# Optimization experiments

Measured on AMD Instinct MI355X. Metric: run time of the kernel, lower is better.

Reference implementation:

```python
import jax, jax.numpy as jnp
import numpy as np

B, T, D = 32, 256, 256  # batch, input_length, output_dim (input_dim == output_dim)
SCALE = 0.06  # ~ 1/sqrt(D) glorot-ish init so LSTM gates don't saturate


def hard_sigmoid(x):
    # Keras-1 default inner_activation for LSTM
    return jnp.clip(0.2 * x + 0.5, 0.0, 1.0)


def lstm_cell(x_t, h, c, W, U, b, d):
    # Keras gate order: i, f, c(g), o
    z = x_t @ W + h @ U + b
    i = hard_sigmoid(z[:, :d])
    f = hard_sigmoid(z[:, d:2 * d])
    g = jnp.tanh(z[:, 2 * d:3 * d])
    o = hard_sigmoid(z[:, 3 * d:])
    c_new = f * c + i * g
    h_new = o * jnp.tanh(c_new)
    return h_new, c_new


def setup_inputs() -> dict:
    key = jax.random.key(0)
    ks = jax.random.split(key, 7)
    x = jax.random.normal(ks[0], (B, T, D), dtype=jnp.float32)
    reader_W = jax.random.normal(ks[1], (D, 4 * D), dtype=jnp.float32) * SCALE
    reader_U = jax.random.normal(ks[2], (D, 4 * D), dtype=jnp.float32) * SCALE
    reader_b = jnp.zeros((4 * D,), jnp.float32)
    writer_W = jax.random.normal(ks[3], (2 * D, 4 * D), dtype=jnp.float32) * SCALE
    writer_U = jax.random.normal(ks[4], (D, 4 * D), dtype=jnp.float32) * SCALE
    writer_b = jnp.zeros((4 * D,), jnp.float32)
    composer_W = jax.random.normal(ks[5], (2 * D, 2 * D), dtype=jnp.float32) * SCALE
    composer_b = jnp.zeros((2 * D,), jnp.float32)
    return {"x": x, "reader_W": reader_W, "reader_U": reader_U, "reader_b": reader_b,
            "writer_W": writer_W, "writer_U": writer_U, "writer_b": writer_b,
            "composer_W": composer_W, "composer_b": composer_b}


def reference(x, reader_W, reader_U, reader_b, writer_W, writer_U, writer_b,
              composer_W, composer_b):
    b, t, d = x.shape
    h0 = jnp.zeros((b, d), x.dtype)
    c0 = jnp.zeros((b, d), x.dtype)

    # ---- read: reader LSTM over the sequence (return_sequences) ----
    def rstep(carry, x_t):
        h, c = carry
        h, c = lstm_cell(x_t, h, c, reader_W, reader_U, reader_b, d)
        return (h, c), h

    _, o_seq = jax.lax.scan(rstep, (h0, c0), jnp.swapaxes(x, 0, 1))  # [T,B,D]

    mem0 = x  # mem_0 = input (B, T, D)

    # ---- compose_and_write_step per timestep ----
    def step(carry, o_t):
        mem, wh, wc = carry
        # summarize_memory: eqs 2-3
        scores = jnp.einsum('bd,btd->bt', o_t, mem)
        z_t = jax.nn.softmax(scores, axis=-1)                 # (B, T)
        m_rt = jnp.einsum('bt,btd->bd', z_t, mem)             # (B, D)
        # compose (eq 4), linear activation
        c_t = jnp.concatenate([o_t, m_rt], axis=-1) @ composer_W + composer_b  # (B, 2D)
        # writer LSTM step (eq 5)
        wh, wc = lstm_cell(c_t, wh, wc, writer_W, writer_U, writer_b, d)
        # update_memory (eq 6): blend via tiled z_t / h_t
        zt = z_t[:, :, None]
        mem = mem * (1.0 - zt) + wh[:, None, :] * zt
        return (mem, wh, wc), wh

    (_, _, _), hs = jax.lax.scan(step, (mem0, h0, c0), o_seq)  # hs: [T,B,D]
    return hs[-1]  # return_mode == 'last_output'
```

## Files before the change

kernel.cpp:

```cpp
#include <hip/hip_runtime.h>
#include <math.h>

#define TB 512
#define NBATCH 32
#define TT 256
#define DD 256

typedef float f32x4 __attribute__((ext_vector_type(4)));

#define WS_WF   0u
#define WS_BF   524288u
#define WS_HP   525312u
#define WS_PAR  541696u
#define PS      260
#define WS_WHP  608256u
#define WS_BAR  616448u
#define WS_FLOATS 624704u

#define O_WW    0
#define S_WW    792
#define O_RW    12672
#define S_RW    524
#define O_MEM   21056
#define S_MEM   260
#define O_WACT  29376
#define S_WACT  792
#define O_RACT  35712
#define S_RACT  524
#define O_WZ    39904
#define O_RZ    40064
#define O_SS    40224
#define O_SE    40256
#define O_WC    40288
#define O_RC    40320
#define O_WB    40352
#define O_RB    40368
#define O_RJ    40384
#define O_MS    40448
#define LDS_FLOATS 40576
#define DYN_LDS_BYTES (LDS_FLOATS*4)

__device__ __forceinline__ float hsig(float x) { return fminf(fmaxf(0.2f*x + 0.5f, 0.f), 1.f); }
__device__ __forceinline__ int ak(int k) { return k + 4*(k/128); }

__device__ __forceinline__ void gst(float* p, float v) {
  __hip_atomic_store(p, v, __ATOMIC_RELAXED, __HIP_MEMORY_SCOPE_AGENT);
}
__device__ __forceinline__ float gld(const float* p) {
  return __hip_atomic_load(p, __ATOMIC_RELAXED, __HIP_MEMORY_SCOPE_AGENT);
}
__device__ __forceinline__ void gst4(float* p, f32x4 v) {
  asm volatile("global_store_dwordx4 %0, %1, off sc0 sc1" :: "v"(p), "v"(v) : "memory");
}

__device__ __forceinline__ void bar_arrive(int* myflag, int phase) {
  asm volatile("s_waitcnt vmcnt(0) lgkmcnt(0)" ::: "memory");
  __syncthreads();
  if (threadIdx.x == 0)
    __hip_atomic_store(myflag, phase, __ATOMIC_RELAXED, __HIP_MEMORY_SCOPE_AGENT);
}
__device__ __forceinline__ void bar_wait(int* flags, int phase) {
  if (threadIdx.x < 64) {
    int sp = 0;
    for (;;) {
      const int v = __hip_atomic_load(&flags[threadIdx.x*32], __ATOMIC_RELAXED,
                                      __HIP_MEMORY_SCOPE_AGENT);
      if (__all(v >= phase)) break;
      if (++sp > (1 << 16)) break;
    }
  }
  __syncthreads();
}
__device__ __forceinline__ void barrier_fenced(int* cnt, int target) {
  __syncthreads();
  if (threadIdx.x == 0) {
    __threadfence();
    __hip_atomic_fetch_add(cnt, 1, __ATOMIC_RELAXED, __HIP_MEMORY_SCOPE_AGENT);
    int sp = 0;
    while (__hip_atomic_load(cnt, __ATOMIC_RELAXED, __HIP_MEMORY_SCOPE_AGENT) < target) {
      if (++sp > (1 << 20)) break;
    }
    __threadfence();
  }
  __syncthreads();
}

__global__ void __launch_bounds__(TB) nse_kernel(
    const float* __restrict__ x,
    const float* __restrict__ rW, const float* __restrict__ rU, const float* __restrict__ rb,
    const float* __restrict__ wW, const float* __restrict__ wU, const float* __restrict__ wb,
    const float* __restrict__ cW, const float* __restrict__ cb,
    float* __restrict__ out, float* __restrict__ ws)
{
  extern __shared__ float sm[];
  const int tid = threadIdx.x;
  const int w = blockIdx.x;
  const int g = w >> 6;
  const int m = w & 63;
  const int b0 = g * 8;
  const int blm = m >> 3;
  const int isl = m & 7;
  const int bmy = b0 + blm;

  float* Wf   = ws + WS_WF;
  float* bfv  = ws + WS_BF;
  float* hpub = ws + WS_HP;
  float* par  = ws + WS_PAR;
  float* whp  = ws + WS_WHP;
  int*   bars = (int*)(ws + WS_BAR);
  int* flg    = &bars[g*2048];
  int* myflag = &bars[g*2048 + m*32];
  int* lcnt   = &bars[8192];
  int* magic  = &bars[8192 + 32];

  if (w == 0 && tid == 0) {
    __hip_atomic_store(lcnt, 0, __ATOMIC_RELAXED, __HIP_MEMORY_SCOPE_AGENT);
    __hip_atomic_store(magic, 1357911, __ATOMIC_RELEASE, __HIP_MEMORY_SCOPE_AGENT);
  }
  if (tid == 0) {
    int sp = 0;
    while (__hip_atomic_load(magic, __ATOMIC_ACQUIRE, __HIP_MEMORY_SCOPE_AGENT) != 1357911) {
      if (++sp > (1 << 20)) break;
    }
  }
  __syncthreads();

  {
    const int kt = w >> 4, nt = w & 15;
    const int r = tid >> 4, c4 = (tid & 15) * 4;
    float a0 = 0.f, a1 = 0.f, a2 = 0.f, a3 = 0.f;
    for (int jc = 0; jc < 512; jc += 32) {
      for (int u = tid; u < 1024; u += TB) {
        int rr = u >> 5, jj = u & 31;
        sm[rr*33 + jj] = cW[(32*kt + rr)*512 + jc + jj];
      }
      {
        int jj = tid >> 4, cc = (tid & 15) * 4;
        const f32x4 v = *(const f32x4*)&wW[(jc + jj)*1024 + 64*nt + cc];
        float* d = &sm[1056 + jj*68 + cc];
        d[0] = v.x; d[1] = v.y; d[2] = v.z; d[3] = v.w;
      }
      __syncthreads();
      #pragma unroll 8
      for (int j = 0; j < 32; j++) {
        const float a = sm[r*33 + j];
        const float* wv = &sm[1056 + j*68 + c4];
        a0 += a*wv[0]; a1 += a*wv[1]; a2 += a*wv[2]; a3 += a*wv[3];
      }
      __syncthreads();
    }
    float* d = &Wf[(32*kt + r)*1024 + 64*nt + c4];
    d[0] = a0; d[1] = a1; d[2] = a2; d[3] = a3;
  }
  if (w >= 16 && w < 32) {
    __syncthreads();
    const int base = (w - 16) * 64;
    const int c = tid & 63, jq = tid >> 6;
    float p = 0.f;
    for (int j = 64*jq; j < 64*jq + 64; j++) p += cb[j] * wW[j*1024 + base + c];
    sm[jq*68 + c] = p;
    __syncthreads();
    if (tid < 64) {
      float s = wb[base + tid];
      for (int j = 0; j < 8; j++) s += sm[j*68 + tid];
      bfv[base + tid] = s;
    }
  }
  barrier_fenced(lcnt, 256);

  for (int u = tid; u < 3072; u += TB) {
    const int k = u >> 2, gate = u & 3;
    const float* sp = (k < 512) ? &Wf[(size_t)k*1024 + gate*256 + 4*m]
                                : &wU[(size_t)(k-512)*1024 + gate*256 + 4*m];
    const f32x4 v = *(const f32x4*)sp;
    const int ik = ak(k);
    sm[O_WW + (gate*4+0)*S_WW + ik] = v.x;
    sm[O_WW + (gate*4+1)*S_WW + ik] = v.y;
    sm[O_WW + (gate*4+2)*S_WW + ik] = v.z;
    sm[O_WW + (gate*4+3)*S_WW + ik] = v.w;
  }
  for (int u = tid; u < 2048; u += TB) {
    const int k = u >> 2, gate = u & 3;
    const float* sp = (k < 256) ? &rW[(size_t)k*1024 + gate*256 + 4*m]
                                : &rU[(size_t)(k-256)*1024 + gate*256 + 4*m];
    const f32x4 v = *(const f32x4*)sp;
    const int ik = ak(k);
    sm[O_RW + (gate*4+0)*S_RW + ik] = v.x;
    sm[O_RW + (gate*4+1)*S_RW + ik] = v.y;
    sm[O_RW + (gate*4+2)*S_RW + ik] = v.z;
    sm[O_RW + (gate*4+3)*S_RW + ik] = v.w;
  }
  for (int u = tid; u < 2048; u += TB) {
    const int r = u >> 6, d4 = (u & 63) * 4;
    *(f32x4*)&sm[O_MEM + r*S_MEM + d4] =
        *(const f32x4*)&x[((size_t)bmy*TT + 32*isl + r)*DD + d4];
  }
  for (int u = tid; u < LDS_FLOATS - O_WACT; u += TB) sm[O_WACT + u] = 0.f;
  {
    const int bl = tid >> 6, d4 = (tid & 63) * 4;
    *(f32x4*)&sm[O_RACT + bl*S_RACT + ak(d4)] =
        *(const f32x4*)&x[(size_t)(b0+bl)*TT*DD + d4];
  }
  if (tid < 16) {
    const int gate = tid >> 2, dl = tid & 3;
    sm[O_WB + tid] = bfv[gate*256 + 4*m + dl];
    sm[O_RB + tid] = rb[gate*256 + 4*m + dl];
  }
  __syncthreads();

  const int q  = tid & 3;
  const int cl = ((tid >> 4) & 3) + 4 * (tid >> 7);
  const int bl8 = ((tid >> 2) & 3) + 4 * ((tid >> 6) & 1);
  const int qo = (q >> 1) * 132 + (q & 1) * 64;

  int bphase = 0;
  for (int s = 0; s <= TT; s++) {
    {
      const int bl = tid >> 6, d4 = (tid & 63) * 4;
      f32x4 vh, vw;
      const float* ph = &hpub[(size_t)((s+1)&1)*8192 + (b0+bl)*256 + d4];
      const float* pw = &whp[(b0+bl)*256 + d4];
      asm volatile(
        "global_load_dwordx4 %0, %2, off sc0 sc1\n\t"
        "global_load_dwordx4 %1, %3, off sc0 sc1\n\t"
        "s_waitcnt vmcnt(0)"
        : "=&v"(vh), "=&v"(vw) : "v"(ph), "v"(pw) : "memory");
      if (s >= 1) {
        *(f32x4*)&sm[O_RACT + bl*S_RACT + ak(256 + d4)] = vh;
        *(f32x4*)&sm[O_WACT + bl*S_WACT + ak(d4)]       = vh;
      }
      if (s >= 2)
        *(f32x4*)&sm[O_WACT + bl*S_WACT + ak(512 + d4)] = vw;
    }
    __syncthreads();

    if (s >= 1) {
      const int r = tid >> 4, tk = tid & 15;
      float* mrow = &sm[O_MEM + r*S_MEM + 16*tk];
      const float* orow = &sm[O_RACT + blm*S_RACT + ak(256 + 16*tk)];
      float acc = 0.f;
      if (s >= 2) {
        const float zr = sm[O_SE + r] * sm[O_RJ + blm*8 + isl];
        const float omz = 1.f - zr;
        const float* hrow = &sm[O_WACT + blm*S_WACT + ak(512 + 16*tk)];
        #pragma unroll
        for (int i2 = 0; i2 < 16; i2 += 4) {
          f32x4 mv = *(f32x4*)(mrow + i2);
          const f32x4 hv = *(const f32x4*)(hrow + i2);
          const f32x4 ov = *(const f32x4*)(orow + i2);
          mv.x = mv.x*omz + hv.x*zr;  mv.y = mv.y*omz + hv.y*zr;
          mv.z = mv.z*omz + hv.z*zr;  mv.w = mv.w*omz + hv.w*zr;
          *(f32x4*)(mrow + i2) = mv;
          acc += mv.x*ov.x + mv.y*ov.y + mv.z*ov.z + mv.w*ov.w;
        }
      } else {
        #pragma unroll
        for (int i2 = 0; i2 < 16; i2 += 4) {
          const f32x4 mv = *(const f32x4*)(mrow + i2);
          const f32x4 ov = *(const f32x4*)(orow + i2);
          acc += mv.x*ov.x + mv.y*ov.y + mv.z*ov.z + mv.w*ov.w;
        }
      }
      acc += __shfl_xor(acc, 1, 64); acc += __shfl_xor(acc, 2, 64);
      acc += __shfl_xor(acc, 4, 64); acc += __shfl_xor(acc, 8, 64);
      if (tk == 0) sm[O_SS + r] = acc;
    }
    __syncthreads();
    if (s >= 1 && tid < 32) {
      const float sc = sm[O_SS + tid];
      float mx = sc;
      mx = fmaxf(mx, __shfl_xor(mx, 1, 64)); mx = fmaxf(mx, __shfl_xor(mx, 2, 64));
      mx = fmaxf(mx, __shfl_xor(mx, 4, 64)); mx = fmaxf(mx, __shfl_xor(mx, 8, 64));
      mx = fmaxf(mx, __shfl_xor(mx, 16, 64));
      const float e = __expf(sc - mx);
      float su = e;
      su += __shfl_xor(su, 1, 64); su += __shfl_xor(su, 2, 64); su += __shfl_xor(su, 4, 64);
      su += __shfl_xor(su, 8, 64); su += __shfl_xor(su, 16, 64);
      sm[O_SE + tid] = e;
      if (tid == 0) {
        gst(&par[((size_t)bmy*8 + isl)*PS + 256], mx);
        gst(&par[((size_t)bmy*8 + isl)*PS + 257], su);
      }
    }
    __syncthreads();
    if (s >= 1) {
      const int dblk = tid >> 3, rh = tid & 7;
      f32x4 p; p.x = 0.f; p.y = 0.f; p.z = 0.f; p.w = 0.f;
      #pragma unroll
      for (int i = 0; i < 4; i++) {
        const int rr = 4*rh + i;
        const float e = sm[O_SE + rr];
        const f32x4 mv = *(const f32x4*)&sm[O_MEM + rr*S_MEM + 4*dblk];
        p.x += e*mv.x; p.y += e*mv.y; p.z += e*mv.z; p.w += e*mv.w;
      }
      p.x += __shfl_xor(p.x,1,64); p.x += __shfl_xor(p.x,2,64); p.x += __shfl_xor(p.x,4,64);
      p.y += __shfl_xor(p.y,1,64); p.y += __shfl_xor(p.y,2,64); p.y += __shfl_xor(p.y,4,64);
      p.z += __shfl_xor(p.z,1,64); p.z += __shfl_xor(p.z,2,64); p.z += __shfl_xor(p.z,4,64);
      p.w += __shfl_xor(p.w,1,64); p.w += __shfl_xor(p.w,2,64); p.w += __shfl_xor(p.w,4,64);
      if (rh == 0) gst4(&par[((size_t)bmy*8 + isl)*PS + 4*dblk], p);
    }
    ++bphase; bar_arrive(myflag, bphase);

    float accw = 0.f;
    if (s <= TT-1) {
      const float* wr = &sm[O_RW + cl*S_RW + 132*q];
      const float* ar = &sm[O_RACT + bl8*S_RACT + 132*q];
      float acc = 0.f;
      #pragma unroll
      for (int kk = 0; kk < 128; kk += 4) {
        const f32x4 wv = *(const f32x4*)(wr + kk);
        const f32x4 av = *(const f32x4*)(ar + kk);
        acc += wv.x*av.x + wv.y*av.y + wv.z*av.z + wv.w*av.w;
      }
      acc += __shfl_xor(acc, 1, 64);
      acc += __shfl_xor(acc, 2, 64);
      if (q == 0) sm[O_RZ + bl8*20 + cl] = acc + sm[O_RB + cl];
    }
    if (s >= 1) {
      const float* wr = &sm[O_WW + cl*S_WW];
      const float* ar = &sm[O_WACT + bl8*S_WACT];
      #pragma unroll
      for (int kk = 0; kk < 64; kk += 4) {
        const f32x4 w0 = *(const f32x4*)(wr + qo + kk);
        const f32x4 a0 = *(const f32x4*)(ar + qo + kk);
        const f32x4 w2 = *(const f32x4*)(wr + 528 + qo + kk);
        const f32x4 a2 = *(const f32x4*)(ar + 528 + qo + kk);
        accw += w0.x*a0.x + w0.y*a0.y + w0.z*a0.z + w0.w*a0.w;
        accw += w2.x*a2.x + w2.y*a2.y + w2.z*a2.z + w2.w*a2.w;
      }
    }
    __syncthreads();
    if (s <= TT-1 && tid < 32) {
      const int bl = tid >> 2, dl = tid & 3;
      const float zi = sm[O_RZ + bl*20 + dl];
      const float zf = sm[O_RZ + bl*20 + 4 + dl];
      const float zg = sm[O_RZ + bl*20 + 8 + dl];
      const float zo = sm[O_RZ + bl*20 + 12 + dl];
      const float cn = hsig(zf)*sm[O_RC + tid] + hsig(zi)*tanhf(zg);
      sm[O_RC + tid] = cn;
      gst(&hpub[(size_t)(s&1)*8192 + (b0+bl)*256 + 4*m + dl], hsig(zo)*tanhf(cn));
    }
    bar_wait(flg, bphase);

    if (s >= 1) {
      const int bl = tid >> 6, d4 = (tid & 63) * 4;
      f32x4 v0,v1,v2,v3,v4,v5,v6,v7;
      float msv;
      {
        const float* p0 = &par[((size_t)(b0+bl)*8 + 0)*PS + d4];
        const float* p4 = p0 + 4*PS;
        const int idx = tid & 127;
        const float* msp = &par[((size_t)(b0 + (idx>>4))*8 + ((idx>>1)&7))*PS + 256 + (idx&1)];
        asm volatile(
          "global_load_dwordx4 %0, %9, off sc0 sc1\n\t"
          "global_load_dwordx4 %1, %9, off offset:1040 sc0 sc1\n\t"
          "global_load_dwordx4 %2, %9, off offset:2080 sc0 sc1\n\t"
          "global_load_dwordx4 %3, %9, off offset:3120 sc0 sc1\n\t"
          "global_load_dwordx4 %4, %10, off sc0 sc1\n\t"
          "global_load_dwordx4 %5, %10, off offset:1040 sc0 sc1\n\t"
          "global_load_dwordx4 %6, %10, off offset:2080 sc0 sc1\n\t"
          "global_load_dwordx4 %7, %10, off offset:3120 sc0 sc1\n\t"
          "global_load_dword   %8, %11, off sc0 sc1\n\t"
          "s_waitcnt vmcnt(0)"
          : "=&v"(v0),"=&v"(v1),"=&v"(v2),"=&v"(v3),
            "=&v"(v4),"=&v"(v5),"=&v"(v6),"=&v"(v7),"=&v"(msv)
          : "v"(p0), "v"(p4), "v"(msp) : "memory");
      }
      if (tid < 128) sm[O_MS + tid] = msv;
      __syncthreads();
      if (tid < 8) {
        const int bl2 = tid;
        float M = sm[O_MS + bl2*16];
        for (int j = 1; j < 8; j++) M = fmaxf(M, sm[O_MS + bl2*16 + 2*j]);
        float tot = 0.f, f0[8];
        for (int j = 0; j < 8; j++) {
          f0[j] = __expf(sm[O_MS + bl2*16 + 2*j] - M);
          tot += f0[j] * sm[O_MS + bl2*16 + 2*j + 1];
        }
        const float inv = 1.f / tot;
        for (int j = 0; j < 8; j++) sm[O_RJ + bl2*8 + j] = f0[j]*inv;
      }
      __syncthreads();
      {
        const float* rj = &sm[O_RJ + bl*8];
        f32x4 a;
        a.x = rj[0]*v0.x + rj[1]*v1.x + rj[2]*v2.x + rj[3]*v3.x
            + rj[4]*v4.x + rj[5]*v5.x + rj[6]*v6.x + rj[7]*v7.x;
        a.y = rj[0]*v0.y + rj[1]*v1.y + rj[2]*v2.y + rj[3]*v3.y
            + rj[4]*v4.y + rj[5]*v5.y + rj[6]*v6.y + rj[7]*v7.y;
        a.z = rj[0]*v0.z + rj[1]*v1.z + rj[2]*v2.z + rj[3]*v3.z
            + rj[4]*v4.z + rj[5]*v5.z + rj[6]*v6.z + rj[7]*v7.z;
        a.w = rj[0]*v0.w + rj[1]*v1.w + rj[2]*v2.w + rj[3]*v3.w
            + rj[4]*v4.w + rj[5]*v5.w + rj[6]*v6.w + rj[7]*v7.w;
        *(f32x4*)&sm[O_WACT + bl*S_WACT + ak(256 + d4)] = a;
      }
      __syncthreads();
      {
        const float* wr = &sm[O_WW + cl*S_WW + 264 + qo];
        const float* ar = &sm[O_WACT + bl8*S_WACT + 264 + qo];
        #pragma unroll
        for (int kk = 0; kk < 64; kk += 4) {
          const f32x4 wv = *(const f32x4*)(wr + kk);
          const f32x4 av = *(const f32x4*)(ar + kk);
          accw += wv.x*av.x + wv.y*av.y + wv.z*av.z + wv.w*av.w;
        }
        accw += __shfl_xor(accw, 1, 64);
        accw += __shfl_xor(accw, 2, 64);
        if (q == 0) sm[O_WZ + bl8*20 + cl] = accw + sm[O_WB + cl];
      }
      __syncthreads();
      if (tid < 32) {
        const int bl2 = tid >> 2, dl = tid & 3;
        const float zi = sm[O_WZ + bl2*20 + dl];
        const float zf = sm[O_WZ + bl2*20 + 4 + dl];
        const float zg = sm[O_WZ + bl2*20 + 8 + dl];
        const float zo = sm[O_WZ + bl2*20 + 12 + dl];
        const float cn = hsig(zf)*sm[O_WC + tid] + hsig(zi)*tanhf(zg);
        sm[O_WC + tid] = cn;
        const float hn = hsig(zo)*tanhf(cn);
        if (s == TT) out[(b0+bl2)*256 + 4*m + dl] = hn;
        else         gst(&whp[(b0+bl2)*256 + 4*m + dl], hn);
      }
    }
    if (s == TT) break;
    ++bphase; bar_arrive(myflag, bphase);
    if (s <= TT-2) {
      const int bl = tid >> 6, d4 = (tid & 63) * 4;
      *(f32x4*)&sm[O_RACT + bl*S_RACT + ak(d4)] =
          *(const f32x4*)&x[((size_t)(b0+bl)*TT + s + 1)*DD + d4];
    }
    bar_wait(flg, bphase);
  }
}

extern "C" void kernel_launch(void* const* d_in, const int* in_sizes, int n_in,
                              void* d_out, int out_size, void* d_ws, size_t ws_size,
                              hipStream_t stream) {
  (void)in_sizes; (void)n_in;
  if (ws_size < (size_t)WS_FLOATS * 4u) {
    hipMemsetAsync(d_out, 0, (size_t)out_size * 4u, stream);
    return;
  }
  const float* x  = (const float*)d_in[0];
  const float* rW = (const float*)d_in[1];
  const float* rU = (const float*)d_in[2];
  const float* rb = (const float*)d_in[3];
  const float* wW = (const float*)d_in[4];
  const float* wU = (const float*)d_in[5];
  const float* wb = (const float*)d_in[6];
  const float* cW = (const float*)d_in[7];
  const float* cb = (const float*)d_in[8];
  float* out = (float*)d_out;
  float* ws  = (float*)d_ws;

  hipFuncSetAttribute((const void*)nse_kernel,
                      hipFuncAttributeMaxDynamicSharedMemorySize, DYN_LDS_BYTES);

  void* args[] = { (void*)&x, (void*)&rW, (void*)&rU, (void*)&rb,
                   (void*)&wW, (void*)&wU, (void*)&wb, (void*)&cW, (void*)&cb,
                   (void*)&out, (void*)&ws };
  hipError_t err = hipLaunchCooperativeKernel((const void*)nse_kernel,
                                              dim3(256), dim3(TB), args,
                                              DYN_LDS_BYTES, stream);
  if (err != hipSuccess) {
    nse_kernel<<<dim3(256), dim3(TB), DYN_LDS_BYTES, stream>>>(
        x, rW, rU, rb, wW, wU, wb, cW, cb, out, ws);
  }
}
```

Baseline: 3.154 ms.

## Split group barriers into two tag channels and defer writer matvec after attention

Replaces the two per-step phase barriers (arrive then wait) with two tag arrays. Each block publishes a tag after its memory partials and after its writer step, and spins only right before it consumes the data that tag guards. The writer h@U part of the matvec is no longer overlapped before the barrier. It is folded into one 192-wide-per-lane dot product after attention, with a matching LDS padding change. tanhf is replaced by an exp-based fast tanh, and the spin loop adds s_sleep and a lower iteration cap. The aim is less barrier stall and some overlap between the reader step and the spin, at the risk of tag races, sleep latency and small precision drift.

```diff
diff --git a/kernel.cpp b/kernel.cpp
--- a/kernel.cpp
+++ b/kernel.cpp
@@ -18,55 +18,60 @@
 #define WS_FLOATS 624704u
 
 #define O_WW    0
-#define S_WW    792
-#define O_RW    12672
+#define S_WW    784
+#define O_RW    12544
 #define S_RW    524
-#define O_MEM   21056
+#define O_MEM   20928
 #define S_MEM   260
-#define O_WACT  29376
+#define O_WACT  29248
 #define S_WACT  792
-#define O_RACT  35712
+#define O_RACT  35584
 #define S_RACT  524
-#define O_WZ    39904
-#define O_RZ    40064
-#define O_SS    40224
-#define O_SE    40256
-#define O_WC    40288
-#define O_RC    40320
-#define O_WB    40352
-#define O_RB    40368
-#define O_RJ    40384
-#define O_MS    40448
-#define LDS_FLOATS 40576
+#define O_WZ    39776
+#define O_RZ    39936
+#define O_SS    40096
+#define O_SE    40128
+#define O_WC    40160
+#define O_RC    40192
+#define O_WB    40224
+#define O_RB    40240
+#define O_RJ    40256
+#define O_MS    40320
+#define LDS_FLOATS 40448
 #define DYN_LDS_BYTES (LDS_FLOATS*4)
 
 __device__ __forceinline__ float hsig(float x) { return fminf(fmaxf(0.2f*x + 0.5f, 0.f), 1.f); }
-__device__ __forceinline__ int ak(int k) { return k + 4*(k/128); }
+__device__ __forceinline__ float ftanh(float x) {
+  const float a = fminf(fabsf(x), 15.f);
+  const float e = __expf(2.f * a);
+  const float r = (e - 1.f) / (e + 1.f);
+  return copysignf(r, x);
+}
+__device__ __forceinline__ int akw(int k) { return k + 4*(k/192); }
+__device__ __forceinline__ int akr(int k) { return k + 4*(k/128); }
 
 __device__ __forceinline__ void gst(float* p, float v) {
   __hip_atomic_store(p, v, __ATOMIC_RELAXED, __HIP_MEMORY_SCOPE_AGENT);
 }
-__device__ __forceinline__ float gld(const float* p) {
-  return __hip_atomic_load(p, __ATOMIC_RELAXED, __HIP_MEMORY_SCOPE_AGENT);
-}
 __device__ __forceinline__ void gst4(float* p, f32x4 v) {
   asm volatile("global_store_dwordx4 %0, %1, off sc0 sc1" :: "v"(p), "v"(v) : "memory");
 }
 
-__device__ __forceinline__ void bar_arrive(int* myflag, int phase) {
+__device__ __forceinline__ void tag_store(int* tp, int v) {
   asm volatile("s_waitcnt vmcnt(0) lgkmcnt(0)" ::: "memory");
   __syncthreads();
   if (threadIdx.x == 0)
-    __hip_atomic_store(myflag, phase, __ATOMIC_RELAXED, __HIP_MEMORY_SCOPE_AGENT);
-}
-__device__ __forceinline__ void bar_wait(int* flags, int phase) {
+    __hip_atomic_store(tp, v, __ATOMIC_RELAXED, __HIP_MEMORY_SCOPE_AGENT);
+}
+__device__ __forceinline__ void tag_spin(const int* tags, int v) {
   if (threadIdx.x < 64) {
     int sp = 0;
     for (;;) {
-      const int v = __hip_atomic_load(&flags[threadIdx.x*32], __ATOMIC_RELAXED,
+      const int t = __hip_atomic_load(&tags[threadIdx.x * 16], __ATOMIC_RELAXED,
                                       __HIP_MEMORY_SCOPE_AGENT);
-      if (__all(v >= phase)) break;
-      if (++sp > (1 << 16)) break;
+      if (__all(t == v)) break;
+      __builtin_amdgcn_s_sleep(2);
+      if (++sp > (1 << 14)) break;
     }
   }
   __syncthreads();
@@ -108,8 +113,10 @@
   float* par  = ws + WS_PAR;
   float* whp  = ws + WS_WHP;
   int*   bars = (int*)(ws + WS_BAR);
-  int* flg    = &bars[g*2048];
-  int* myflag = &bars[g*2048 + m*32];
+  int* tagsA  = &bars[g*1024];
+  int* tagsB  = &bars[4096 + g*1024];
+  int* myA    = &tagsA[m*16];
+  int* myB    = &tagsB[m*16];
   int* lcnt   = &bars[8192];
   int* magic  = &bars[8192 + 32];
 
@@ -173,7 +180,7 @@
     const float* sp = (k < 512) ? &Wf[(size_t)k*1024 + gate*256 + 4*m]
                                 : &wU[(size_t)(k-512)*1024 + gate*256 + 4*m];
     const f32x4 v = *(const f32x4*)sp;
-    const int ik = ak(k);
+    const int ik = akw(k);
     sm[O_WW + (gate*4+0)*S_WW + ik] = v.x;
     sm[O_WW + (gate*4+1)*S_WW + ik] = v.y;
     sm[O_WW + (gate*4+2)*S_WW + ik] = v.z;
@@ -184,7 +191,7 @@
     const float* sp = (k < 256) ? &rW[(size_t)k*1024 + gate*256 + 4*m]
                                 : &rU[(size_t)(k-256)*1024 + gate*256 + 4*m];
     const f32x4 v = *(const f32x4*)sp;
-    const int ik = ak(k);
+    const int ik = akr(k);
     sm[O_RW + (gate*4+0)*S_RW + ik] = v.x;
     sm[O_RW + (gate*4+1)*S_RW + ik] = v.y;
     sm[O_RW + (gate*4+2)*S_RW + ik] = v.z;
@@ -196,9 +203,10 @@
         *(const f32x4*)&x[((size_t)bmy*TT + 32*isl + r)*DD + d4];
   }
   for (int u = tid; u < LDS_FLOATS - O_WACT; u += TB) sm[O_WACT + u] = 0.f;
+  __syncthreads();
   {
     const int bl = tid >> 6, d4 = (tid & 63) * 4;
-    *(f32x4*)&sm[O_RACT + bl*S_RACT + ak(d4)] =
+    *(f32x4*)&sm[O_RACT + bl*S_RACT + akr(d4)] =
         *(const f32x4*)&x[(size_t)(b0+bl)*TT*DD + d4];
   }
   if (tid < 16) {
@@ -208,41 +216,38 @@
   }
   __syncthreads();
 
-  const int q  = tid & 3;
-  const int cl = ((tid >> 4) & 3) + 4 * (tid >> 7);
+  const int q   = tid & 3;
+  const int cl  = ((tid >> 4) & 3) + 4 * (tid >> 7);
   const int bl8 = ((tid >> 2) & 3) + 4 * ((tid >> 6) & 1);
-  const int qo = (q >> 1) * 132 + (q & 1) * 64;
-
-  int bphase = 0;
+
   for (int s = 0; s <= TT; s++) {
-    {
+    if (s >= 1) {
+      tag_spin(tagsB, s - 1);
       const int bl = tid >> 6, d4 = (tid & 63) * 4;
       f32x4 vh, vw;
-      const float* ph = &hpub[(size_t)((s+1)&1)*8192 + (b0+bl)*256 + d4];
+      const float* ph = &hpub[(size_t)((s-1)&1)*8192 + (b0+bl)*256 + d4];
       const float* pw = &whp[(b0+bl)*256 + d4];
       asm volatile(
         "global_load_dwordx4 %0, %2, off sc0 sc1\n\t"
         "global_load_dwordx4 %1, %3, off sc0 sc1\n\t"
         "s_waitcnt vmcnt(0)"
         : "=&v"(vh), "=&v"(vw) : "v"(ph), "v"(pw) : "memory");
-      if (s >= 1) {
-        *(f32x4*)&sm[O_RACT + bl*S_RACT + ak(256 + d4)] = vh;
-        *(f32x4*)&sm[O_WACT + bl*S_WACT + ak(d4)]       = vh;
-      }
+      *(f32x4*)&sm[O_RACT + bl*S_RACT + akr(256 + d4)] = vh;
+      *(f32x4*)&sm[O_WACT + bl*S_WACT + akw(d4)]       = vh;
       if (s >= 2)
-        *(f32x4*)&sm[O_WACT + bl*S_WACT + ak(512 + d4)] = vw;
+        *(f32x4*)&sm[O_WACT + bl*S_WACT + akw(512 + d4)] = vw;
     }
     __syncthreads();
 
     if (s >= 1) {
       const int r = tid >> 4, tk = tid & 15;
       float* mrow = &sm[O_MEM + r*S_MEM + 16*tk];
-      const float* orow = &sm[O_RACT + blm*S_RACT + ak(256 + 16*tk)];
+      const float* orow = &sm[O_RACT + blm*S_RACT + akr(256 + 16*tk)];
       float acc = 0.f;
       if (s >= 2) {
         const float zr = sm[O_SE + r] * sm[O_RJ + blm*8 + isl];
         const float omz = 1.f - zr;
-        const float* hrow = &sm[O_WACT + blm*S_WACT + ak(512 + 16*tk)];
+        const float* hrow = &sm[O_WACT + blm*S_WACT + akw(512 + 16*tk)];
         #pragma unroll
         for (int i2 = 0; i2 < 16; i2 += 4) {
           f32x4 mv = *(f32x4*)(mrow + i2);
@@ -298,10 +303,11 @@
       p.z += __shfl_xor(p.z,1,64); p.z += __shfl_xor(p.z,2,64); p.z += __shfl_xor(p.z,4,64);
       p.w += __shfl_xor(p.w,1,64); p.w += __shfl_xor(p.w,2,64); p.w += __shfl_xor(p.w,4,64);
       if (rh == 0) gst4(&par[((size_t)bmy*8 + isl)*PS + 4*dblk], p);
-    }
-    ++bphase; bar_arrive(myflag, bphase);
-
-    float accw = 0.f;
+      tag_store(myA, s);
+    } else {
+      __syncthreads();
+    }
+
     if (s <= TT-1) {
       const float* wr = &sm[O_RW + cl*S_RW + 132*q];
       const float* ar = &sm[O_RACT + bl8*S_RACT + 132*q];
@@ -316,19 +322,6 @@
       acc += __shfl_xor(acc, 2, 64);
       if (q == 0) sm[O_RZ + bl8*20 + cl] = acc + sm[O_RB + cl];
     }
-    if (s >= 1) {
-      const float* wr = &sm[O_WW + cl*S_WW];
-      const float* ar = &sm[O_WACT + bl8*S_WACT];
-      #pragma unroll
-      for (int kk = 0; kk < 64; kk += 4) {
-        const f32x4 w0 = *(const f32x4*)(wr + qo + kk);
-        const f32x4 a0 = *(const f32x4*)(ar + qo + kk);
-        const f32x4 w2 = *(const f32x4*)(wr + 528 + qo + kk);
-        const f32x4 a2 = *(const f32x4*)(ar + 528 + qo + kk);
-        accw += w0.x*a0.x + w0.y*a0.y + w0.z*a0.z + w0.w*a0.w;
-        accw += w2.x*a2.x + w2.y*a2.y + w2.z*a2.z + w2.w*a2.w;
-      }
-    }
     __syncthreads();
     if (s <= TT-1 && tid < 32) {
       const int bl = tid >> 2, dl = tid & 3;
@@ -336,13 +329,13 @@
       const float zf = sm[O_RZ + bl*20 + 4 + dl];
       const float zg = sm[O_RZ + bl*20 + 8 + dl];
       const float zo = sm[O_RZ + bl*20 + 12 + dl];
-      const float cn = hsig(zf)*sm[O_RC + tid] + hsig(zi)*tanhf(zg);
+      const float cn = hsig(zf)*sm[O_RC + tid] + hsig(zi)*ftanh(zg);
       sm[O_RC + tid] = cn;
-      gst(&hpub[(size_t)(s&1)*8192 + (b0+bl)*256 + 4*m + dl], hsig(zo)*tanhf(cn));
-    }
-    bar_wait(flg, bphase);
+      gst(&hpub[(size_t)(s&1)*8192 + (b0+bl)*256 + 4*m + dl], hsig(zo)*ftanh(cn));
+    }
 
     if (s >= 1) {
+      tag_spin(tagsA, s);
       const int bl = tid >> 6, d4 = (tid & 63) * 4;
       f32x4 v0,v1,v2,v3,v4,v5,v6,v7;
       float msv;
@@ -392,21 +385,22 @@
             + rj[4]*v4.z + rj[5]*v5.z + rj[6]*v6.z + rj[7]*v7.z;
         a.w = rj[0]*v0.w + rj[1]*v1.w + rj[2]*v2.w + rj[3]*v3.w
             + rj[4]*v4.w + rj[5]*v5.w + rj[6]*v6.w + rj[7]*v7.w;
-        *(f32x4*)&sm[O_WACT + bl*S_WACT + ak(256 + d4)] = a;
+        *(f32x4*)&sm[O_WACT + bl*S_WACT + akw(256 + d4)] = a;
       }
       __syncthreads();
       {
-        const float* wr = &sm[O_WW + cl*S_WW + 264 + qo];
-        const float* ar = &sm[O_WACT + bl8*S_WACT + 264 + qo];
-        #pragma unroll
-        for (int kk = 0; kk < 64; kk += 4) {
+        const float* wr = &sm[O_WW + cl*S_WW + 196*q];
+        const float* ar = &sm[O_WACT + bl8*S_WACT + 196*q];
+        float acc = 0.f;
+        #pragma unroll 8
+        for (int kk = 0; kk < 192; kk += 4) {
           const f32x4 wv = *(const f32x4*)(wr + kk);
           const f32x4 av = *(const f32x4*)(ar + kk);
-          accw += wv.x*av.x + wv.y*av.y + wv.z*av.z + wv.w*av.w;
+          acc += wv.x*av.x + wv.y*av.y + wv.z*av.z + wv.w*av.w;
         }
-        accw += __shfl_xor(accw, 1, 64);
-        accw += __shfl_xor(accw, 2, 64);
-        if (q == 0) sm[O_WZ + bl8*20 + cl] = accw + sm[O_WB + cl];
+        acc += __shfl_xor(acc, 1, 64);
+        acc += __shfl_xor(acc, 2, 64);
+        if (q == 0) sm[O_WZ + bl8*20 + cl] = acc + sm[O_WB + cl];
       }
       __syncthreads();
       if (tid < 32) {
@@ -415,21 +409,20 @@
         const float zf = sm[O_WZ + bl2*20 + 4 + dl];
         const float zg = sm[O_WZ + bl2*20 + 8 + dl];
         const float zo = sm[O_WZ + bl2*20 + 12 + dl];
-        const float cn = hsig(zf)*sm[O_WC + tid] + hsig(zi)*tanhf(zg);
+        const float cn = hsig(zf)*sm[O_WC + tid] + hsig(zi)*ftanh(zg);
         sm[O_WC + tid] = cn;
-        const float hn = hsig(zo)*tanhf(cn);
+        const float hn = hsig(zo)*ftanh(cn);
         if (s == TT) out[(b0+bl2)*256 + 4*m + dl] = hn;
         else         gst(&whp[(b0+bl2)*256 + 4*m + dl], hn);
       }
     }
     if (s == TT) break;
-    ++bphase; bar_arrive(myflag, bphase);
+    tag_store(myB, s);
     if (s <= TT-2) {
       const int bl = tid >> 6, d4 = (tid & 63) * 4;
-      *(f32x4*)&sm[O_RACT + bl*S_RACT + ak(d4)] =
+      *(f32x4*)&sm[O_RACT + bl*S_RACT + akr(d4)] =
           *(const f32x4*)&x[((size_t)(b0+bl)*TT + s + 1)*DD + d4];
     }
-    bar_wait(flg, bphase);
   }
 }
 
```

Result: faster. 2.980 ms (-5.5%).
